# Optimization experiments

Hardware: AMD Instinct MI355X
Metric: run time of the kernel (lower is better)

## Reference

```python
import jax, jax.numpy as jnp
import numpy as np
import math

N_HEADS = 32
N_KV_HEADS = 8
MAX_SEQ_LEN = 2048


def _rope_cos_sin(seq_len, head_dim, dtype):
    # precompute_freqs_cis: theta=10000, positions 0..seq_len-1 (note: NOT offset by start_pos, faithful to source)
    inv_freq = 1.0 / (10000.0 ** (jnp.arange(0, head_dim, 2, dtype=jnp.float32) / head_dim))
    t = jnp.arange(seq_len, dtype=jnp.float32)
    angles = jnp.outer(t, inv_freq)  # [S, hd/2]
    return jnp.cos(angles).astype(dtype), jnp.sin(angles).astype(dtype)


def _apply_rope(x, cos, sin):
    # x: [B, S, H, hd]; rotate consecutive pairs (llama complex convention)
    B, S, H, hd = x.shape
    xr = x.reshape(B, S, H, hd // 2, 2)
    x1, x2 = xr[..., 0], xr[..., 1]
    c = cos[None, :, None, :]
    s = sin[None, :, None, :]
    o1 = x1 * c - x2 * s
    o2 = x1 * s + x2 * c
    return jnp.stack([o1, o2], axis=-1).reshape(B, S, H, hd)


def setup_inputs() -> dict:
    key = jax.random.key(0)
    ks = jax.random.split(key, 5)
    dim = 4096
    B, S = 1, 2048
    sd = 1.0 / math.sqrt(dim)
    return {
        "x": jax.random.normal(ks[0], (B, S, dim), dtype=jnp.float32),
        "wq": jax.random.normal(ks[1], (4096, 4096), dtype=jnp.float32) * sd,
        "wk": jax.random.normal(ks[2], (1024, 4096), dtype=jnp.float32) * sd,
        "wv": jax.random.normal(ks[3], (1024, 4096), dtype=jnp.float32) * sd,
        "wo": jax.random.normal(ks[4], (4096, 4096), dtype=jnp.float32) * sd,
        "start_pos": 0,
    }


def reference(x, wq, wk, wv, wo, start_pos):
    B, S, D = x.shape
    Hq, Hkv = N_HEADS, N_KV_HEADS
    hd = D // Hq
    n_rep = Hq // Hkv

    xq = (x @ wq.T).reshape(B, S, Hq, hd)
    xk = (x @ wk.T).reshape(B, S, Hkv, hd)
    xv = (x @ wv.T).reshape(B, S, Hkv, hd)

    cos, sin = _rope_cos_sin(S, hd, x.dtype)
    xq = _apply_rope(xq, cos, sin)
    xk = _apply_rope(xk, cos, sin)

    # KV cache append + read back [:, :start_pos+S] (start_pos is a static Python int)
    cache_k = jnp.zeros((B, MAX_SEQ_LEN, Hkv, hd), dtype=x.dtype)
    cache_v = jnp.zeros((B, MAX_SEQ_LEN, Hkv, hd), dtype=x.dtype)
    cache_k = jax.lax.dynamic_update_slice(cache_k, xk, (0, start_pos, 0, 0))
    cache_v = jax.lax.dynamic_update_slice(cache_v, xv, (0, start_pos, 0, 0))
    kv_len = start_pos + S
    keys = cache_k[:, :kv_len]    # [B, K, Hkv, hd]
    values = cache_v[:, :kv_len]

    # GQA repeat_kv: [B, K, Hkv, hd] -> [B, K, Hq, hd]
    keys = jnp.broadcast_to(keys[:, :, :, None, :], (B, kv_len, Hkv, n_rep, hd)).reshape(B, kv_len, Hq, hd)
    values = jnp.broadcast_to(values[:, :, :, None, :], (B, kv_len, Hkv, n_rep, hd)).reshape(B, kv_len, Hq, hd)

    scale = 1.0 / math.sqrt(hd)
    scores = jnp.einsum('bqhd,bkhd->bhqk', xq, keys) * scale  # [B, Hq, S, K]
    # NOTE: source applies NO causal mask — faithful reproduction
    attn = jax.nn.softmax(scores, axis=-1)
    out = jnp.einsum('bhqk,bkhd->bqhd', attn, values).reshape(B, S, Hq * hd)
    return out @ wo.T
```

## Files before the change

### kernel.cpp

```cpp
#include <hip/hip_runtime.h>
#include <hip/hip_bf16.h>

typedef _Float16 f16_t;
typedef unsigned int uint;
typedef __attribute__((ext_vector_type(8))) _Float16 f16x8;
typedef __attribute__((ext_vector_type(4))) _Float16 f16x4;
typedef __attribute__((ext_vector_type(4))) float f32x4;
typedef __attribute__((ext_vector_type(16))) float f32x16;

#define ROPE_C (13.287712379549449f / 64.0f)

__global__ __launch_bounds__(256) void repack_all(const float* __restrict__ x,
                                                  const float* __restrict__ wq,
                                                  const float* __restrict__ wk,
                                                  const float* __restrict__ wv,
                                                  const float* __restrict__ wo,
                                                  uint16_t* __restrict__ xh,
                                                  uint16_t* __restrict__ wqkv,
                                                  uint16_t* __restrict__ woh)
{
    const int bid = blockIdx.x;
    const int tid = threadIdx.x;
    const int k4 = tid & 7;
    const int slot = k4 >> 1;
    const int so   = (k4 & 1) * 4;

    if (bid < 2048) {
        const int p  = bid >> 7;
        const int kb = bid & 127;
        const int rr = tid >> 3;
        uint16_t* bh = xh + ((size_t)p * 128 + kb) * 4096;
        #pragma unroll
        for (int it = 0; it < 4; ++it) {
            const int r = it * 32 + rr;
            const float4 v = *reinterpret_cast<const float4*>(
                &x[((size_t)p * 128 + r) * 4096 + kb * 32 + k4 * 4]);
            float f[4] = {v.x, v.y, v.z, v.w};
            f16x4 h;
            #pragma unroll
            for (int e = 0; e < 4; ++e) h[e] = (f16_t)f[e];
            const int pos = r * 32 + ((slot ^ ((r >> 1) & 3)) << 3) + so;
            *reinterpret_cast<f16x4*>(&bh[pos]) = h;
        }
    } else if (bid < 10240) {
        const int idx = bid - 2048;
        const int pan = idx >> 7;
        const int kb  = idx & 127;
        uint16_t* bh = wqkv + ((size_t)pan * 128 + kb) * 3072;
        #pragma unroll
        for (int it = 0; it < 3; ++it) {
            const int r = it * 32 + (tid >> 3);
            const int n = pan * 96 + r;
            const float* srow = (n < 4096) ? (wq + (size_t)n * 4096)
                              : (n < 5120) ? (wk + (size_t)(n - 4096) * 4096)
                                           : (wv + (size_t)(n - 5120) * 4096);
            const float4 v = *reinterpret_cast<const float4*>(srow + kb * 32 + k4 * 4);
            float f[4] = {v.x, v.y, v.z, v.w};
            f16x4 h;
            #pragma unroll
            for (int e = 0; e < 4; ++e) h[e] = (f16_t)f[e];
            const int pos = r * 32 + ((slot ^ ((r >> 1) & 3)) << 3) + so;
            *reinterpret_cast<f16x4*>(&bh[pos]) = h;
        }
    } else {
        const int idx = bid - 10240;
        const int p  = idx >> 7;
        const int kb = idx & 127;
        const int rr = tid >> 3;
        uint16_t* bh = woh + ((size_t)p * 128 + kb) * 4096;
        #pragma unroll
        for (int it = 0; it < 4; ++it) {
            const int r = it * 32 + rr;
            const float4 v = *reinterpret_cast<const float4*>(
                &wo[((size_t)p * 128 + r) * 4096 + kb * 32 + k4 * 4]);
            float f[4] = {v.x, v.y, v.z, v.w};
            f16x4 h;
            #pragma unroll
            for (int e = 0; e < 4; ++e) h[e] = (f16_t)f[e];
            const int pos = r * 32 + ((slot ^ ((r >> 1) & 3)) << 3) + so;
            *reinterpret_cast<f16x4*>(&bh[pos]) = h;
        }
    }
}

__global__ __launch_bounds__(512) void gemm_qkv9(const uint16_t* __restrict__ xh,
                                                 const uint16_t* __restrict__ wqkv,
                                                 uint16_t* __restrict__ xq16,
                                                 uint16_t* __restrict__ xk16,
                                                 uint16_t* __restrict__ xv16)
{
    __shared__ char lds[2][40960];

    const int bid = blockIdx.x;
    const int xcd = bid & 7;
    const int i_  = bid >> 3;
    const int by = (xcd & 1) * 8 + (i_ & 7);
    const int bx = (xcd >> 1) * 8 + (i_ >> 3);
    const int tid = threadIdx.x;
    const int w = tid >> 6, lane = tid & 63;
    const int wm = w >> 2, wn = w & 3;
    const int fr = lane & 15, s4 = lane >> 4;

    const uint16_t* sp[5];
    int dof[5];
    int stridec[5];
    #pragma unroll
    for (int i = 0; i < 5; ++i) {
        const int c = w + 8 * i;
        if (c < 16) {
            const int kk = c >> 3, inner = c & 7;
            sp[i] = xh + (size_t)by * 524288 + kk * 4096 + inner * 512 + lane * 8;
            dof[i] = c * 1024;
            stridec[i] = 8192;
        } else {
            const int cb = c - 16;
            const int pan = cb / 12, rem = cb % 12;
            const int kk = rem / 6, inner = rem % 6;
            sp[i] = wqkv + (size_t)(bx * 2 + pan) * 393216 + kk * 3072 + inner * 512 + lane * 8;
            dof[i] = 16384 + cb * 1024;
            stridec[i] = 6144;
        }
    }

    f32x4 acc[4][3] = {};

    #pragma unroll
    for (int i = 0; i < 5; ++i)
        __builtin_amdgcn_global_load_lds(
            (const __attribute__((address_space(1))) void*)(sp[i]),
            (__attribute__((address_space(3))) void*)(&lds[0][0] + dof[i]), 16, 0, 0);
    asm volatile("s_waitcnt vmcnt(0)" ::: "memory");
    __builtin_amdgcn_s_barrier();
    __builtin_amdgcn_sched_barrier(0);

    for (int t = 0; t < 64; ++t) {
        const char* b = &lds[t & 1][0];
        if (t + 1 < 64) {
            char* nb = &lds[(t + 1) & 1][0];
            #pragma unroll
            for (int i = 0; i < 5; ++i)
                __builtin_amdgcn_global_load_lds(
                    (const __attribute__((address_space(1))) void*)(sp[i] + (size_t)(t + 1) * stridec[i]),
                    (__attribute__((address_space(3))) void*)(nb + dof[i]), 16, 0, 0);
        }
        #pragma unroll
        for (int kk = 0; kk < 2; ++kk) {
            f16x8 fb[3];
            #pragma unroll
            for (int j = 0; j < 3; ++j) {
                const int cbp = wn * 48 + j * 16 + fr;
                const int pan = (cbp >= 96) ? 1 : 0;
                const int rb = cbp - pan * 96;
                fb[j] = *reinterpret_cast<const f16x8*>(
                    b + 16384 + pan * 12288 + kk * 6144 + rb * 64 + ((s4 ^ ((rb >> 1) & 3)) << 4));
            }
            #pragma unroll
            for (int ri = 0; ri < 4; ++ri) {
                const int rloc = wm * 64 + ri * 16 + fr;
                f16x8 fh = *reinterpret_cast<const f16x8*>(
                    b + kk * 8192 + rloc * 64 + ((s4 ^ ((rloc >> 1) & 3)) << 4));
                __builtin_amdgcn_s_setprio(1);
                #pragma unroll
                for (int j = 0; j < 3; ++j)
                    acc[ri][j] = __builtin_amdgcn_mfma_f32_16x16x32_f16(fh, fb[j], acc[ri][j], 0, 0, 0);
                __builtin_amdgcn_s_setprio(0);
            }
        }
        asm volatile("s_waitcnt vmcnt(0)" ::: "memory");
        __builtin_amdgcn_s_barrier();
        __builtin_amdgcn_sched_barrier(0);
    }

    const int r0 = by * 128 + wm * 64 + s4 * 4;
    const int c0 = bx * 192 + wn * 48 + fr;
    #pragma unroll
    for (int ri = 0; ri < 4; ++ri)
        #pragma unroll
        for (int j = 0; j < 3; ++j) {
            const int col = c0 + j * 16;
            #pragma unroll
            for (int rr = 0; rr < 4; ++rr) {
                const int row = r0 + ri * 16 + rr;
                const f16_t v = (f16_t)acc[ri][j][rr];
                uint16_t bits;
                __builtin_memcpy(&bits, &v, 2);
                if (col < 4096)      xq16[(size_t)row * 4096 + col] = bits;
                else if (col < 5120) xk16[(size_t)row * 1024 + (col - 4096)] = bits;
                else                 xv16[(size_t)row * 1024 + (col - 5120)] = bits;
            }
        }
}

__global__ __launch_bounds__(512) void gemm_out8(const uint16_t* __restrict__ aoh,
                                                 const uint16_t* __restrict__ woh,
                                                 float* __restrict__ out)
{
    __shared__ char lds[2][49152];

    const int bid = blockIdx.x;
    const int xcd = bid & 7;
    const int i_  = bid >> 3;
    const int by = (xcd & 1) * 4 + (i_ & 3);
    const int bx = (xcd >> 1) * 8 + (i_ >> 2);
    const int tid = threadIdx.x;
    const int w = tid >> 6, lane = tid & 63;
    const int wm = w >> 2, wn = w & 3;
    const int fr = lane & 15, s4 = lane >> 4;

    const uint16_t* sp[6];
    int dof[6];
    #pragma unroll
    for (int i = 0; i < 6; ++i) {
        const int c = w + 8 * i;
        if (c < 32) {
            const int pan = c >> 4, sub = c & 15;
            sp[i] = aoh + (size_t)(2 * by + pan) * 524288 + sub * 512 + lane * 8;
            dof[i] = c * 1024;
        } else {
            sp[i] = woh + (size_t)bx * 524288 + (c - 32) * 512 + lane * 8;
            dof[i] = 32768 + (c - 32) * 1024;
        }
    }

    f32x4 acc[8][2] = {};

    #pragma unroll
    for (int i = 0; i < 6; ++i)
        __builtin_amdgcn_global_load_lds(
            (const __attribute__((address_space(1))) void*)(sp[i]),
            (__attribute__((address_space(3))) void*)(&lds[0][0] + dof[i]), 16, 0, 0);
    asm volatile("s_waitcnt vmcnt(0)" ::: "memory");
    __builtin_amdgcn_s_barrier();
    __builtin_amdgcn_sched_barrier(0);

    for (int t = 0; t < 64; ++t) {
        const char* b = &lds[t & 1][0];
        if (t + 1 < 64) {
            char* nb = &lds[(t + 1) & 1][0];
            #pragma unroll
            for (int i = 0; i < 6; ++i)
                __builtin_amdgcn_global_load_lds(
                    (const __attribute__((address_space(1))) void*)(sp[i] + (size_t)(t + 1) * 8192),
                    (__attribute__((address_space(3))) void*)(nb + dof[i]), 16, 0, 0);
        }
        #pragma unroll
        for (int kk = 0; kk < 2; ++kk) {
            f16x8 fb[2];
            #pragma unroll
            for (int j = 0; j < 2; ++j) {
                const int cbp = wn * 32 + j * 16 + fr;
                fb[j] = *reinterpret_cast<const f16x8*>(
                    b + 32768 + kk * 8192 + cbp * 64 + ((s4 ^ ((cbp >> 1) & 3)) << 4));
            }
            #pragma unroll
            for (int p = 0; p < 4; ++p) {
                f16x8 fh[2];
                #pragma unroll
                for (int f = 0; f < 2; ++f) {
                    const int rloc = p * 32 + f * 16 + fr;
                    fh[f] = *reinterpret_cast<const f16x8*>(
                        b + wm * 16384 + kk * 8192 + rloc * 64 + ((s4 ^ ((rloc >> 1) & 3)) << 4));
                }
                __builtin_amdgcn_s_setprio(1);
                #pragma unroll
                for (int f = 0; f < 2; ++f)
                    #pragma unroll
                    for (int j = 0; j < 2; ++j)
                        acc[p * 2 + f][j] = __builtin_amdgcn_mfma_f32_16x16x32_f16(fh[f], fb[j], acc[p * 2 + f][j], 0, 0, 0);
                __builtin_amdgcn_s_setprio(0);
            }
        }
        asm volatile("s_waitcnt vmcnt(0)" ::: "memory");
        __builtin_amdgcn_s_barrier();
        __builtin_amdgcn_sched_barrier(0);
    }

    const int r0 = by * 256 + wm * 128 + s4 * 4;
    const int c0 = bx * 128 + wn * 32 + fr;
    #pragma unroll
    for (int ri = 0; ri < 8; ++ri)
        #pragma unroll
        for (int j = 0; j < 2; ++j)
            #pragma unroll
            for (int rr = 0; rr < 4; ++rr)
                out[(size_t)(r0 + ri * 16 + rr) * 4096 + c0 + j * 16] = acc[ri][j][rr];
}

__global__ __launch_bounds__(256) void conv_kv(const uint16_t* __restrict__ xk16,
                                               const uint16_t* __restrict__ xv16,
                                               uint16_t* __restrict__ kvg)
{
    __shared__ float V[32][129];
    const int t = blockIdx.x;
    const int h = blockIdx.y;
    const int tid = threadIdx.x;
    uint16_t* tile = kvg + ((size_t)(h * 64 + t)) * 8192;

    #pragma unroll
    for (int i = 0; i < 4; ++i) {
        const int v = i * 256 + tid;
        const int row = v >> 5, c4 = (v & 31) * 4;
        f16x4 hv = *reinterpret_cast<const f16x4*>(&xv16[(size_t)(t * 32 + row) * 1024 + h * 128 + c4]);
        #pragma unroll
        for (int e = 0; e < 4; ++e) V[row][c4 + e] = (float)hv[e];
    }

    {
        const int r = tid >> 3;
        const int d0 = (tid & 7) * 16;
        const int pos_ = t * 32 + r;
        float f[16];
        const uint16_t* kr = &xk16[(size_t)pos_ * 1024 + h * 128 + d0];
        f16x8 k0 = *reinterpret_cast<const f16x8*>(kr);
        f16x8 k1 = *reinterpret_cast<const f16x8*>(kr + 8);
        #pragma unroll
        for (int e = 0; e < 8; ++e) { f[e] = (float)k0[e]; f[8 + e] = (float)k1[e]; }
        #pragma unroll
        for (int i = 0; i < 8; ++i) {
            const int j = (d0 >> 1) + i;
            const float invf = exp2f(-(float)j * ROPE_C);
            const float ang = (float)pos_ * invf;
            float sn, cs;
            __sincosf(ang, &sn, &cs);
            const float x1 = f[2 * i], x2 = f[2 * i + 1];
            f[2 * i]     = x1 * cs - x2 * sn;
            f[2 * i + 1] = x1 * sn + x2 * cs;
        }
        #pragma unroll
        for (int cc = 0; cc < 2; ++cc) {
            f16x8 hv;
            #pragma unroll
            for (int e = 0; e < 8; ++e) hv[e] = (f16_t)f[cc * 8 + e];
            const int c = (d0 >> 3) + cc;
            const int pos = r * 128 + ((c ^ (r & 15)) << 3);
            *reinterpret_cast<f16x8*>(&tile[pos]) = hv;
        }
    }
    __syncthreads();
    {
        const int d = tid >> 1;
        const int k0 = (tid & 1) * 16;
        float g[16];
        #pragma unroll
        for (int j = 0; j < 16; ++j) g[j] = V[k0 + j][d];
        #pragma unroll
        for (int cc = 0; cc < 2; ++cc) {
            f16x8 hv;
            #pragma unroll
            for (int e = 0; e < 8; ++e) hv[e] = (f16_t)g[cc * 8 + e];
            const int c = (k0 >> 3) + cc;
            const int pos = 4096 + d * 32 + ((c ^ ((d >> 1) & 3)) << 3);
            *reinterpret_cast<f16x8*>(&tile[pos]) = hv;
        }
    }
}

__device__ __forceinline__ uint cvtpkh(float lo, float hi) {
    uint r;
    asm("v_cvt_pkrtz_f16_f32 %0, %1, %2" : "=v"(r) : "v"(lo), "v"(hi));
    return r;
}
__device__ __forceinline__ void permswap(uint& a, uint& b) {
    asm("v_permlane32_swap_b32 %0, %1" : "+v"(a), "+v"(b));
}
__device__ __forceinline__ f16x8 pack4h(uint w0, uint w1, uint w2, uint w3) {
    union { uint u[4]; f16x8 v; } t;
    t.u[0] = w0; t.u[1] = w1; t.u[2] = w2; t.u[3] = w3;
    return t.v;
}

__global__ __launch_bounds__(512, 2) void attn_mfma(const uint16_t* __restrict__ xq16,
                                                    const uint16_t* __restrict__ kvg,
                                                    uint16_t* __restrict__ aoh)
{
    __shared__ char lds[3][16384];

    const int b = blockIdx.x;
    const int kvh = b & 7;
    const int r = b >> 3;
    const int h = kvh * 4 + (r & 3);
    const int q0 = (r >> 2) * 256;
    const int tid = threadIdx.x;
    const int w = tid >> 6;
    const int lane = tid & 63;
    const int ln31 = lane & 31;
    const int hi = lane >> 5;

    const int q = q0 + w * 32 + ln31;
    const uint16_t* qrow = xq16 + (size_t)q * 4096 + h * 128;
    f16x8 Qh[8];
    #pragma unroll
    for (int ks = 0; ks < 8; ++ks) {
        const int dbase = ks * 16 + hi * 8;
        f16x8 raw = *reinterpret_cast<const f16x8*>(qrow + dbase);
        float f[8];
        #pragma unroll
        for (int e = 0; e < 8; ++e) f[e] = (float)raw[e];
        #pragma unroll
        for (int i = 0; i < 4; ++i) {
            const int j = (dbase >> 1) + i;
            const float invf = exp2f(-(float)j * ROPE_C);
            const float ang = (float)q * invf;
            float sn, cs;
            __sincosf(ang, &sn, &cs);
            const float x1 = f[2 * i], x2 = f[2 * i + 1];
            f[2 * i]     = (x1 * cs - x2 * sn) * 0.08838834764831845f;
            f[2 * i + 1] = (x1 * sn + x2 * cs) * 0.08838834764831845f;
        }
        #pragma unroll
        for (int e = 0; e < 8; ++e) Qh[ks][e] = (f16_t)f[e];
    }

    const char* gkv = (const char*)kvg + (size_t)kvh * 64 * 16384;

    f32x16 oacc[4] = {{}, {}, {}, {}};
    float m = -3.0e38f, l = 0.f;

    #pragma unroll
    for (int tt = 0; tt < 2; ++tt) {
        const char* g = gkv + (size_t)tt * 16384;
        #pragma unroll
        for (int i = 0; i < 2; ++i) {
            const int chunk = i * 8 + w;
            __builtin_amdgcn_global_load_lds(
                (const __attribute__((address_space(1))) void*)(g + chunk * 1024 + lane * 16),
                (__attribute__((address_space(3))) void*)(&lds[tt][chunk * 1024]),
                16, 0, 0);
        }
    }

    int cur = 0;
    for (int t = 0; t < 64; ++t) {
        if (t + 1 < 64) asm volatile("s_waitcnt vmcnt(2)" ::: "memory");
        else            asm volatile("s_waitcnt vmcnt(0)" ::: "memory");
        __builtin_amdgcn_s_barrier();
        __builtin_amdgcn_sched_barrier(0);
        if (t + 2 < 64) {
            int nb = cur + 2; if (nb >= 3) nb -= 3;
            const char* g = gkv + (size_t)(t + 2) * 16384;
            #pragma unroll
            for (int i = 0; i < 2; ++i) {
                const int chunk = i * 8 + w;
                __builtin_amdgcn_global_load_lds(
                    (const __attribute__((address_space(1))) void*)(g + chunk * 1024 + lane * 16),
                    (__attribute__((address_space(3))) void*)(&lds[nb][chunk * 1024]),
                    16, 0, 0);
            }
        }
        const char* Kf = &lds[cur][0];
        const char* Vf = &lds[cur][0] + 8192;

        f32x16 s0 = {}, s1 = {};
        __builtin_amdgcn_s_setprio(1);
        #pragma unroll
        for (int ks = 0; ks < 8; ++ks) {
            const int byt = ln31 * 256 + ((ks * 32 + hi * 16) ^ ((ln31 & 15) << 4));
            f16x8 a = *reinterpret_cast<const f16x8*>(Kf + byt);
            if (ks & 1) s1 = __builtin_amdgcn_mfma_f32_32x32x16_f16(a, Qh[ks], s1, 0, 0, 0);
            else        s0 = __builtin_amdgcn_mfma_f32_32x32x16_f16(a, Qh[ks], s0, 0, 0, 0);
        }
        __builtin_amdgcn_s_setprio(0);
        f32x16 s = s0 + s1;

        float pmax = s[0];
        #pragma unroll
        for (int jj = 1; jj < 16; ++jj) pmax = fmaxf(pmax, s[jj]);
        pmax = fmaxf(pmax, __shfl_xor(pmax, 32));
        if (!__all(pmax - m <= 8.0f)) {
            const float mnew = fmaxf(m, pmax);
            const float corr = __expf(m - mnew);
            l *= corr;
            #pragma unroll
            for (int dt = 0; dt < 4; ++dt) oacc[dt] *= corr;
            m = mnew;
        }
        float psum = 0.f;
        #pragma unroll
        for (int jj = 0; jj < 16; ++jj) {
            float pv = __expf(s[jj] - m);
            s[jj] = pv;
            psum += pv;
        }
        psum += __shfl_xor(psum, 32);
        l += psum;

        #pragma unroll
        for (int ks = 0; ks < 2; ++ks) {
            const int b0 = ks * 8;
            uint wa = cvtpkh(s[b0 + 0], s[b0 + 1]);
            uint wb = cvtpkh(s[b0 + 2], s[b0 + 3]);
            uint wc = cvtpkh(s[b0 + 4], s[b0 + 5]);
            uint wd = cvtpkh(s[b0 + 6], s[b0 + 7]);
            permswap(wa, wc); permswap(wb, wd);
            f16x8 Pf = pack4h(wa, wb, wc, wd);
            __builtin_amdgcn_s_setprio(1);
            #pragma unroll
            for (int dt = 0; dt < 4; ++dt) {
                const int row = dt * 32 + ln31;
                const int byt = row * 64 + ((ks * 32 + hi * 16) ^ (((row >> 1) & 3) << 4));
                f16x8 vh = *reinterpret_cast<const f16x8*>(Vf + byt);
                oacc[dt] = __builtin_amdgcn_mfma_f32_32x32x16_f16(vh, Pf, oacc[dt], 0, 0, 0);
            }
            __builtin_amdgcn_s_setprio(0);
        }
        if (++cur == 3) cur = 0;
    }

    const float invl = 1.0f / l;
    const int p   = q >> 7;
    const int rr_ = q & 127;
    const int rsw = (rr_ >> 1) & 3;
    #pragma unroll
    for (int dt = 0; dt < 4; ++dt) {
        const int kb = h * 4 + dt;
        uint16_t* bh = aoh + ((size_t)p * 128 + kb) * 4096;
        #pragma unroll
        for (int g4 = 0; g4 < 4; ++g4) {
            f16x4 hv;
            #pragma unroll
            for (int e = 0; e < 4; ++e)
                hv[e] = (f16_t)(oacc[dt][g4 * 4 + e] * invl);
            const int pos = rr_ * 32 + ((g4 ^ rsw) << 3) + 4 * hi;
            *reinterpret_cast<f16x4*>(&bh[pos]) = hv;
        }
    }
}

extern "C" void kernel_launch(void* const* d_in, const int* in_sizes, int n_in,
                              void* d_out, int out_size, void* d_ws, size_t ws_size,
                              hipStream_t stream)
{
    const float* x  = (const float*)d_in[0];
    const float* wq = (const float*)d_in[1];
    const float* wk = (const float*)d_in[2];
    const float* wv = (const float*)d_in[3];
    const float* wo = (const float*)d_in[4];
    float* out = (float*)d_out;

    float* ws = (float*)d_ws;
    uint16_t* xq16 = (uint16_t*)ws;
    uint16_t* kvg  = (uint16_t*)(ws + 8388608);
    uint16_t* xk16 = (uint16_t*)(ws + 12582912);
    uint16_t* xv16 = (uint16_t*)(ws + 14680064);
    uint16_t* aoh  = (uint16_t*)(ws + 12582912);
    uint16_t* xh   = (uint16_t*)(ws + 20971520);
    uint16_t* wqkv = (uint16_t*)(ws + 29360128);
    uint16_t* woh  = (uint16_t*)(ws + 41943040);

    dim3 blk(256);
    repack_all<<<dim3(14336), blk, 0, stream>>>(x, wq, wk, wv, wo, xh, wqkv, woh);
    gemm_qkv9 <<<dim3(512), dim3(512), 0, stream>>>(xh, wqkv, xq16, xk16, xv16);
    conv_kv   <<<dim3(64, 8), blk, 0, stream>>>(xk16, xv16, kvg);
    attn_mfma <<<dim3(256), dim3(512), 0, stream>>>(xq16, kvg, aoh);
    gemm_out8 <<<dim3(256), dim3(512), 0, stream>>>(aoh, woh, out);
}
```

Measured before the change: 342.3 us.

## Software-pipeline attention loop so QK of next tile overlaps softmax and PV

```diff
diff --git a/kernel.cpp b/kernel.cpp
--- a/kernel.cpp
+++ b/kernel.cpp
@@ -369,11 +369,11 @@
     return t.v;
 }
 
-__global__ __launch_bounds__(512, 2) void attn_mfma(const uint16_t* __restrict__ xq16,
+__global__ __launch_bounds__(512, 1) void attn_mfma(const uint16_t* __restrict__ xq16,
                                                     const uint16_t* __restrict__ kvg,
                                                     uint16_t* __restrict__ aoh)
 {
-    __shared__ char lds[3][16384];
+    __shared__ char lds[4][16384];
 
     const int b = blockIdx.x;
     const int kvh = b & 7;
@@ -415,6 +415,86 @@
 
     f32x16 oacc[4] = {{}, {}, {}, {}};
     float m = -3.0e38f, l = 0.f;
+    f32x16 s0A, s1A, s0B, s1B;
+
+#define WAIT_STAGE(T_) do {                                                         \
+        if ((T_) + 1 < 64) asm volatile("s_waitcnt vmcnt(2)" ::: "memory");          \
+        else               asm volatile("s_waitcnt vmcnt(0)" ::: "memory");          \
+        __builtin_amdgcn_s_barrier();                                                \
+        __builtin_amdgcn_sched_barrier(0);                                           \
+        if ((T_) + 2 < 64) {                                                         \
+            const char* g_ = gkv + (size_t)((T_) + 2) * 16384;                       \
+            char* dst_ = &lds[((T_) + 2) & 3][0];                                    \
+            _Pragma("unroll")                                                        \
+            for (int i_ = 0; i_ < 2; ++i_) {                                         \
+                const int chunk_ = i_ * 8 + w;                                       \
+                __builtin_amdgcn_global_load_lds(                                    \
+                    (const __attribute__((address_space(1))) void*)(g_ + chunk_ * 1024 + lane * 16), \
+                    (__attribute__((address_space(3))) void*)(dst_ + chunk_ * 1024), \
+                    16, 0, 0);                                                       \
+            }                                                                        \
+        }                                                                            \
+    } while (0)
+
+#define QK_TILE(T_, S0_, S1_) do {                                                  \
+        const char* Kf_ = &lds[(T_) & 3][0];                                        \
+        S0_ = (f32x16){};                                                           \
+        S1_ = (f32x16){};                                                           \
+        __builtin_amdgcn_s_setprio(1);                                              \
+        _Pragma("unroll")                                                           \
+        for (int ks_ = 0; ks_ < 8; ++ks_) {                                         \
+            const int byt_ = ln31 * 256 + ((ks_ * 32 + hi * 16) ^ ((ln31 & 15) << 4)); \
+            f16x8 a_ = *reinterpret_cast<const f16x8*>(Kf_ + byt_);                 \
+            if (ks_ & 1) S1_ = __builtin_amdgcn_mfma_f32_32x32x16_f16(a_, Qh[ks_], S1_, 0, 0, 0); \
+            else         S0_ = __builtin_amdgcn_mfma_f32_32x32x16_f16(a_, Qh[ks_], S0_, 0, 0, 0); \
+        }                                                                           \
+        __builtin_amdgcn_s_setprio(0);                                              \
+    } while (0)
+
+#define SMPV_TILE(T_, S0_, S1_) do {                                                \
+        const char* Vf_ = &lds[(T_) & 3][0] + 8192;                                 \
+        f32x16 s_ = S0_ + S1_;                                                      \
+        float pmax_ = s_[0];                                                        \
+        _Pragma("unroll")                                                           \
+        for (int jj_ = 1; jj_ < 16; ++jj_) pmax_ = fmaxf(pmax_, s_[jj_]);           \
+        pmax_ = fmaxf(pmax_, __shfl_xor(pmax_, 32));                                \
+        if (!__all(pmax_ - m <= 8.0f)) {                                            \
+            const float mnew_ = fmaxf(m, pmax_);                                    \
+            const float corr_ = __expf(m - mnew_);                                  \
+            l *= corr_;                                                             \
+            _Pragma("unroll")                                                       \
+            for (int dt_ = 0; dt_ < 4; ++dt_) oacc[dt_] *= corr_;                   \
+            m = mnew_;                                                              \
+        }                                                                           \
+        float psum_ = 0.f;                                                          \
+        _Pragma("unroll")                                                           \
+        for (int jj_ = 0; jj_ < 16; ++jj_) {                                        \
+            float pv_ = __expf(s_[jj_] - m);                                        \
+            s_[jj_] = pv_;                                                          \
+            psum_ += pv_;                                                           \
+        }                                                                           \
+        psum_ += __shfl_xor(psum_, 32);                                             \
+        l += psum_;                                                                 \
+        _Pragma("unroll")                                                           \
+        for (int ks_ = 0; ks_ < 2; ++ks_) {                                         \
+            const int b0_ = ks_ * 8;                                                \
+            uint wa_ = cvtpkh(s_[b0_ + 0], s_[b0_ + 1]);                            \
+            uint wb_ = cvtpkh(s_[b0_ + 2], s_[b0_ + 3]);                            \
+            uint wc_ = cvtpkh(s_[b0_ + 4], s_[b0_ + 5]);                            \
+            uint wd_ = cvtpkh(s_[b0_ + 6], s_[b0_ + 7]);                            \
+            permswap(wa_, wc_); permswap(wb_, wd_);                                 \
+            f16x8 Pf_ = pack4h(wa_, wb_, wc_, wd_);                                 \
+            __builtin_amdgcn_s_setprio(1);                                          \
+            _Pragma("unroll")                                                       \
+            for (int dt_ = 0; dt_ < 4; ++dt_) {                                     \
+                const int row_ = dt_ * 32 + ln31;                                   \
+                const int byt_ = row_ * 64 + ((ks_ * 32 + hi * 16) ^ (((row_ >> 1) & 3) << 4)); \
+                f16x8 vh_ = *reinterpret_cast<const f16x8*>(Vf_ + byt_);            \
+                oacc[dt_] = __builtin_amdgcn_mfma_f32_32x32x16_f16(vh_, Pf_, oacc[dt_], 0, 0, 0); \
+            }                                                                       \
+            __builtin_amdgcn_s_setprio(0);                                          \
+        }                                                                           \
+    } while (0)
 
     #pragma unroll
     for (int tt = 0; tt < 2; ++tt) {
@@ -429,82 +509,24 @@
         }
     }
 
-    int cur = 0;
-    for (int t = 0; t < 64; ++t) {
-        if (t + 1 < 64) asm volatile("s_waitcnt vmcnt(2)" ::: "memory");
-        else            asm volatile("s_waitcnt vmcnt(0)" ::: "memory");
-        __builtin_amdgcn_s_barrier();
-        __builtin_amdgcn_sched_barrier(0);
-        if (t + 2 < 64) {
-            int nb = cur + 2; if (nb >= 3) nb -= 3;
-            const char* g = gkv + (size_t)(t + 2) * 16384;
-            #pragma unroll
-            for (int i = 0; i < 2; ++i) {
-                const int chunk = i * 8 + w;
-                __builtin_amdgcn_global_load_lds(
-                    (const __attribute__((address_space(1))) void*)(g + chunk * 1024 + lane * 16),
-                    (__attribute__((address_space(3))) void*)(&lds[nb][chunk * 1024]),
-                    16, 0, 0);
-            }
-        }
-        const char* Kf = &lds[cur][0];
-        const char* Vf = &lds[cur][0] + 8192;
-
-        f32x16 s0 = {}, s1 = {};
-        __builtin_amdgcn_s_setprio(1);
-        #pragma unroll
-        for (int ks = 0; ks < 8; ++ks) {
-            const int byt = ln31 * 256 + ((ks * 32 + hi * 16) ^ ((ln31 & 15) << 4));
-            f16x8 a = *reinterpret_cast<const f16x8*>(Kf + byt);
-            if (ks & 1) s1 = __builtin_amdgcn_mfma_f32_32x32x16_f16(a, Qh[ks], s1, 0, 0, 0);
-            else        s0 = __builtin_amdgcn_mfma_f32_32x32x16_f16(a, Qh[ks], s0, 0, 0, 0);
-        }
-        __builtin_amdgcn_s_setprio(0);
-        f32x16 s = s0 + s1;
-
-        float pmax = s[0];
-        #pragma unroll
-        for (int jj = 1; jj < 16; ++jj) pmax = fmaxf(pmax, s[jj]);
-        pmax = fmaxf(pmax, __shfl_xor(pmax, 32));
-        if (!__all(pmax - m <= 8.0f)) {
-            const float mnew = fmaxf(m, pmax);
-            const float corr = __expf(m - mnew);
-            l *= corr;
-            #pragma unroll
-            for (int dt = 0; dt < 4; ++dt) oacc[dt] *= corr;
-            m = mnew;
-        }
-        float psum = 0.f;
-        #pragma unroll
-        for (int jj = 0; jj < 16; ++jj) {
-            float pv = __expf(s[jj] - m);
-            s[jj] = pv;
-            psum += pv;
-        }
-        psum += __shfl_xor(psum, 32);
-        l += psum;
-
-        #pragma unroll
-        for (int ks = 0; ks < 2; ++ks) {
-            const int b0 = ks * 8;
-            uint wa = cvtpkh(s[b0 + 0], s[b0 + 1]);
-            uint wb = cvtpkh(s[b0 + 2], s[b0 + 3]);
-            uint wc = cvtpkh(s[b0 + 4], s[b0 + 5]);
-            uint wd = cvtpkh(s[b0 + 6], s[b0 + 7]);
-            permswap(wa, wc); permswap(wb, wd);
-            f16x8 Pf = pack4h(wa, wb, wc, wd);
-            __builtin_amdgcn_s_setprio(1);
-            #pragma unroll
-            for (int dt = 0; dt < 4; ++dt) {
-                const int row = dt * 32 + ln31;
-                const int byt = row * 64 + ((ks * 32 + hi * 16) ^ (((row >> 1) & 3) << 4));
-                f16x8 vh = *reinterpret_cast<const f16x8*>(Vf + byt);
-                oacc[dt] = __builtin_amdgcn_mfma_f32_32x32x16_f16(vh, Pf, oacc[dt], 0, 0, 0);
-            }
-            __builtin_amdgcn_s_setprio(0);
-        }
-        if (++cur == 3) cur = 0;
-    }
+    WAIT_STAGE(0);
+    QK_TILE(0, s0A, s1A);
+
+    for (int tp = 1; tp < 64; tp += 2) {
+        WAIT_STAGE(tp);
+        QK_TILE(tp, s0B, s1B);
+        SMPV_TILE(tp - 1, s0A, s1A);
+        if (tp + 1 < 64) {
+            WAIT_STAGE(tp + 1);
+            QK_TILE(tp + 1, s0A, s1A);
+            SMPV_TILE(tp, s0B, s1B);
+        }
+    }
+    SMPV_TILE(63, s0B, s1B);
+
+#undef WAIT_STAGE
+#undef QK_TILE
+#undef SMPV_TILE
 
     const float invl = 1.0f / l;
     const int p   = q >> 7;
```

Result: no change. 340.0 us (-0.7%).
